# Performance work log

Measured on AMD Instinct MI355X. Metric: run time of the kernel, lower is better.

## Reference

```python
import jax, jax.numpy as jnp
import numpy as np

THRESH_SCALE = 0.05

def ste_ternary(w):
    # forward: quantize to {-1,0,+1}; backward: straight-through (identity)
    thr = THRESH_SCALE * jnp.mean(jnp.abs(w))
    q = jnp.where(w > thr, 1.0, jnp.where(w < -thr, -1.0, 0.0)).astype(w.dtype)
    return w + jax.lax.stop_gradient(q - w)

def setup_inputs() -> dict:
    key = jax.random.key(0)
    kx, kw = jax.random.split(key)
    x = jax.random.normal(kx, (8192, 4096), dtype=jnp.float32)
    weight = jax.random.normal(kw, (4096, 4096), dtype=jnp.float32) * 0.1
    return {"x": x, "weight": weight}

def reference(x, weight):
    w_t = ste_ternary(weight)          # [out, in] in {-1,0,+1}
    return x @ w_t.T                    # [tokens, out]
```

## Files before the change

kernel.cpp:

```cpp
#include <hip/hip_runtime.h>
#include <hip/hip_bf16.h>
#include <stdint.h>


typedef __attribute__((ext_vector_type(4))) int i32x4;

#define KDIM 4096
#define NDIM 4096

#define M_ROWS 8192
#define ABS_BLOCKS 1024

__device__ inline void gld_lds16(const void* g, void* l) {
  __builtin_amdgcn_global_load_lds(
      (__attribute__((address_space(1))) void*)g,
      (__attribute__((address_space(3))) void*)l,
      16, 0, 0);
}

__device__ inline int pack4(int a, int b, int c, int d) {
  return (a & 255) | ((b & 255) << 8) | ((c & 255) << 16) | (d << 24);
}

__device__ inline int q8(float v, float inv) {
  int q = __float2int_rn(v * inv);
  return q > 127 ? 127 : (q < -127 ? -127 : q);
}

__global__ __launch_bounds__(256) void prep_kernel(
    const float4* __restrict__ x, signed char* __restrict__ xq,
    float* __restrict__ steps, const float4* __restrict__ w, int wn4,
    double* __restrict__ sum) {
  if (blockIdx.x < M_ROWS) {
    const int row = blockIdx.x;
    const float4* xr = x + (size_t)row * 1024;
    float4 v[4];
    float amax = 0.0f;
#pragma unroll
    for (int j = 0; j < 4; ++j) {
      v[j] = xr[threadIdx.x + 256 * j];
      amax = fmaxf(amax, fmaxf(fmaxf(fabsf(v[j].x), fabsf(v[j].y)),
                               fmaxf(fabsf(v[j].z), fabsf(v[j].w))));
    }
#pragma unroll
    for (int off = 32; off > 0; off >>= 1)
      amax = fmaxf(amax, __shfl_down(amax, off, 64));
    __shared__ float wmax[4];
    const int lane = threadIdx.x & 63, wave = threadIdx.x >> 6;
    if (lane == 0) wmax[wave] = amax;
    __syncthreads();
    const float m = fmaxf(fmaxf(wmax[0], wmax[1]), fmaxf(wmax[2], wmax[3]));
    const float inv = m > 0.0f ? 127.0f / m : 0.0f;
    if (threadIdx.x == 0) steps[row] = m > 0.0f ? m / 127.0f : 0.0f;
    int* out = (int*)(xq + (size_t)row * 4096);
#pragma unroll
    for (int j = 0; j < 4; ++j) {
      out[threadIdx.x + 256 * j] = pack4(q8(v[j].x, inv), q8(v[j].y, inv),
                                         q8(v[j].z, inv), q8(v[j].w, inv));
    }
  } else {
    double s = 0.0;
    const int stride = ABS_BLOCKS * 256;
    for (int i = (blockIdx.x - M_ROWS) * 256 + threadIdx.x; i < wn4;
         i += stride) {
      float4 v = w[i];
      s += (double)((fabsf(v.x) + fabsf(v.y)) + (fabsf(v.z) + fabsf(v.w)));
    }
#pragma unroll
    for (int off = 32; off > 0; off >>= 1) s += __shfl_down(s, off, 64);
    __shared__ double wsum[4];
    const int lane = threadIdx.x & 63, wave = threadIdx.x >> 6;
    if (lane == 0) wsum[wave] = s;
    __syncthreads();
    if (threadIdx.x == 0) atomicAdd(sum, wsum[0] + wsum[1] + wsum[2] + wsum[3]);
  }
}

__global__ __launch_bounds__(256) void quant_kernel(
    const float4* __restrict__ w, const double* __restrict__ sum,
    int* __restrict__ q, int n4, double inv_n) {
  const float thr = (float)(0.05 * (*sum) * inv_n);
  const int stride = gridDim.x * blockDim.x;
  for (int i = blockIdx.x * blockDim.x + threadIdx.x; i < n4; i += stride) {
    float4 v = w[i];
    int a = v.x > thr ? 1 : (v.x < -thr ? -1 : 0);
    int b = v.y > thr ? 1 : (v.y < -thr ? -1 : 0);
    int c = v.z > thr ? 1 : (v.z < -thr ? -1 : 0);
    int d = v.w > thr ? 1 : (v.w < -thr ? -1 : 0);
    q[i] = pack4(a, b, c, d);
  }
}

#define MFMA_I8 __builtin_amdgcn_mfma_i32_16x16x64_i8

__global__ __launch_bounds__(512, 2) void gemm_i8_8p(
    const signed char* __restrict__ A, const signed char* __restrict__ B,
    const float* __restrict__ steps, float* __restrict__ C, int M) {
  __shared__ unsigned char lds[131072];

  const int tid = threadIdx.x;
  const int lane = tid & 63;
  const int w = tid >> 6;

  const int bm = blockIdx.y * 256;
  const int bn = blockIdx.x * 256;

  const int rL = lane >> 3;
  const int csw = (((lane & 7) ^ rL) << 4);
  const signed char* aBase = A + (size_t)(bm + w * 8 + rL) * KDIM + csw;
  const signed char* bBase = B + (size_t)(bn + w * 8 + rL) * KDIM + csw;
  unsigned char* const ldsA = lds;
  unsigned char* const ldsB = lds + 65536;

  const int fr = lane & 15;
  const int fk = (lane >> 4) * 16;
  const int xr = (lane & 7) << 4;
  const int cc0 = fk ^ xr;
  const int cc1 = (64 + fk) ^ xr;
  const int wm = (w >> 2) * 128;
  const int wn = (w & 3) * 64;
  const int aro = (wm + fr) * 128;
  const int bro = (wn + fr) * 128;

  i32x4 acc[8][4] = {};

  gld_lds16(bBase, ldsB + w * 1024);
  gld_lds16(bBase + (size_t)64 * KDIM, ldsB + 8192 + w * 1024);
  gld_lds16(bBase + (size_t)128 * KDIM, ldsB + 16384 + w * 1024);
  gld_lds16(bBase + (size_t)192 * KDIM, ldsB + 16384 + 8192 + w * 1024);
  gld_lds16(aBase, ldsA + w * 1024);
  gld_lds16(aBase + (size_t)128 * KDIM, ldsA + 16384 + w * 1024);
  gld_lds16(aBase + (size_t)64 * KDIM, ldsA + 8192 + w * 1024);
  gld_lds16(aBase + (size_t)192 * KDIM, ldsA + 16384 + 8192 + w * 1024);
  asm volatile("s_waitcnt vmcnt(2)" ::: "memory");
  __builtin_amdgcn_s_barrier();

  for (int t = 0; t < 32; ++t) {
    const int b = t & 1;
    const bool st = (t < 31);
    const unsigned char* Ab = ldsA + b * 32768;
    const unsigned char* Bb = ldsB + b * 32768;
    unsigned char* An = ldsA + (b ^ 1) * 32768;
    unsigned char* Bn = ldsB + (b ^ 1) * 32768;
    const signed char* aS = aBase + (size_t)(t + 1) * 128;
    const signed char* bS = bBase + (size_t)(t + 1) * 128;

    i32x4 bfr[4][2];

#pragma unroll
    for (int q = 0; q < 4; ++q) {
      if (q == 0) {
#pragma unroll
        for (int ni = 0; ni < 4; ++ni) {
          bfr[ni][0] = *(const i32x4*)(Bb + bro + ni * 2048 + cc0);
          bfr[ni][1] = *(const i32x4*)(Bb + bro + ni * 2048 + cc1);
        }
      }
      i32x4 a00 = *(const i32x4*)(Ab + aro + (2 * q) * 2048 + cc0);
      i32x4 a01 = *(const i32x4*)(Ab + aro + (2 * q) * 2048 + cc1);
      i32x4 a10 = *(const i32x4*)(Ab + aro + (2 * q + 1) * 2048 + cc0);
      i32x4 a11 = *(const i32x4*)(Ab + aro + (2 * q + 1) * 2048 + cc1);

      if (st) {
        if (q == 0) {
          gld_lds16(bS, Bn + w * 1024);
          gld_lds16(bS + (size_t)64 * KDIM, Bn + 8192 + w * 1024);
        } else if (q == 1) {
          gld_lds16(bS + (size_t)128 * KDIM, Bn + 16384 + w * 1024);
          gld_lds16(bS + (size_t)192 * KDIM, Bn + 16384 + 8192 + w * 1024);
        } else if (q == 2) {
          gld_lds16(aS, An + w * 1024);
          gld_lds16(aS + (size_t)128 * KDIM, An + 16384 + w * 1024);
        } else {
          gld_lds16(aS + (size_t)64 * KDIM, An + 8192 + w * 1024);
          gld_lds16(aS + (size_t)192 * KDIM, An + 16384 + 8192 + w * 1024);
        }
      }

      __builtin_amdgcn_s_barrier();
      asm volatile("s_waitcnt lgkmcnt(0)" ::: "memory");
      __builtin_amdgcn_s_setprio(1);
#pragma unroll
      for (int ni = 0; ni < 4; ++ni) {
        acc[2 * q][ni] = MFMA_I8(a00, bfr[ni][0], acc[2 * q][ni], 0, 0, 0);
        acc[2 * q][ni] = MFMA_I8(a01, bfr[ni][1], acc[2 * q][ni], 0, 0, 0);
        acc[2 * q + 1][ni] =
            MFMA_I8(a10, bfr[ni][0], acc[2 * q + 1][ni], 0, 0, 0);
        acc[2 * q + 1][ni] =
            MFMA_I8(a11, bfr[ni][1], acc[2 * q + 1][ni], 0, 0, 0);
      }
      __builtin_amdgcn_s_setprio(0);

      if (q == 1) {
        if (st)
          asm volatile("s_waitcnt vmcnt(4)" ::: "memory");
        else
          asm volatile("s_waitcnt vmcnt(0)" ::: "memory");
      }
      if (q == 3 && st)
        asm volatile("s_waitcnt vmcnt(2)" ::: "memory");
      __builtin_amdgcn_s_barrier();
    }
  }

  const int cn = lane & 15;
  const int cm = (lane >> 4) * 4;
  float stp[8][4];
#pragma unroll
  for (int mi = 0; mi < 8; ++mi)
#pragma unroll
    for (int r = 0; r < 4; ++r)
      stp[mi][r] = steps[bm + wm + mi * 16 + cm + r];
#pragma unroll
  for (int mi = 0; mi < 8; ++mi) {
#pragma unroll
    for (int ni = 0; ni < 4; ++ni) {
#pragma unroll
      for (int r = 0; r < 4; ++r) {
        const int m = bm + wm + mi * 16 + cm + r;
        const int n = bn + wn + ni * 16 + cn;
        C[(size_t)m * NDIM + n] = (float)acc[mi][ni][r] * stp[mi][r];
      }
    }
  }
}

extern "C" void kernel_launch(void* const* d_in, const int* in_sizes, int n_in,
                              void* d_out, int out_size, void* d_ws,
                              size_t ws_size, hipStream_t stream) {
  const float* x = (const float*)d_in[0];
  const float* w = (const float*)d_in[1];
  float* out = (float*)d_out;

  const int K = 4096;
  const int N = 4096;
  const int M = in_sizes[0] / K;
  const int NW = in_sizes[1];

  char* ws = (char*)d_ws;
  double* d_sum = (double*)ws;
  float* steps = (float*)(ws + 256);
  signed char* qb = (signed char*)(ws + 65536);
  signed char* xq = qb + (size_t)N * K;

  hipMemsetAsync(d_sum, 0, sizeof(double), stream);
  prep_kernel<<<M_ROWS + ABS_BLOCKS, 256, 0, stream>>>(
      (const float4*)x, xq, steps, (const float4*)w, NW / 4, d_sum);
  quant_kernel<<<2048, 256, 0, stream>>>((const float4*)w, d_sum, (int*)qb,
                                         NW / 4, 1.0 / NW);
  dim3 grid(N / 256, M / 256);
  gemm_i8_8p<<<grid, 512, 0, stream>>>(xq, qb, steps, out, M);
}
```

Before: 389.2 us.

## Halve GEMM K-tile to 64 with staggered A/B prefetch and smaller LDS

```diff
diff --git a/kernel.cpp b/kernel.cpp
--- a/kernel.cpp
+++ b/kernel.cpp
@@ -93,10 +93,10 @@
 
 #define MFMA_I8 __builtin_amdgcn_mfma_i32_16x16x64_i8
 
-__global__ __launch_bounds__(512, 2) void gemm_i8_8p(
+__global__ __launch_bounds__(512, 4) void gemm_i8_2b(
     const signed char* __restrict__ A, const signed char* __restrict__ B,
     const float* __restrict__ steps, float* __restrict__ C, int M) {
-  __shared__ unsigned char lds[131072];
+  __shared__ unsigned char lds[65536];
 
   const int tid = threadIdx.x;
   const int lane = tid & 63;
@@ -105,102 +105,87 @@
   const int bm = blockIdx.y * 256;
   const int bn = blockIdx.x * 256;
 
-  const int rL = lane >> 3;
-  const int csw = (((lane & 7) ^ rL) << 4);
-  const signed char* aBase = A + (size_t)(bm + w * 8 + rL) * KDIM + csw;
-  const signed char* bBase = B + (size_t)(bn + w * 8 + rL) * KDIM + csw;
+  const int srow = w * 16 + (lane >> 2);
+  const int srcsw = (((lane & 3) ^ ((lane >> 2) & 3) ^ ((lane >> 4) & 3)) << 4);
+  const signed char* aBase = A + (size_t)(bm + srow) * KDIM + srcsw;
+  const signed char* bBase = B + (size_t)(bn + srow) * KDIM + srcsw;
   unsigned char* const ldsA = lds;
-  unsigned char* const ldsB = lds + 65536;
+  unsigned char* const ldsB = lds + 32768;
 
   const int fr = lane & 15;
-  const int fk = (lane >> 4) * 16;
-  const int xr = (lane & 7) << 4;
-  const int cc0 = fk ^ xr;
-  const int cc1 = (64 + fk) ^ xr;
+  const int cc = (((lane >> 4) ^ (lane & 3) ^ ((lane >> 2) & 3)) << 4);
   const int wm = (w >> 2) * 128;
   const int wn = (w & 3) * 64;
-  const int aro = (wm + fr) * 128;
-  const int bro = (wn + fr) * 128;
+  const int aro = (wm + fr) * 64;
+  const int bro = (wn + fr) * 64;
 
   i32x4 acc[8][4] = {};
 
   gld_lds16(bBase, ldsB + w * 1024);
-  gld_lds16(bBase + (size_t)64 * KDIM, ldsB + 8192 + w * 1024);
-  gld_lds16(bBase + (size_t)128 * KDIM, ldsB + 16384 + w * 1024);
-  gld_lds16(bBase + (size_t)192 * KDIM, ldsB + 16384 + 8192 + w * 1024);
+  gld_lds16(bBase + (size_t)128 * KDIM, ldsB + 8192 + w * 1024);
   gld_lds16(aBase, ldsA + w * 1024);
-  gld_lds16(aBase + (size_t)128 * KDIM, ldsA + 16384 + w * 1024);
-  gld_lds16(aBase + (size_t)64 * KDIM, ldsA + 8192 + w * 1024);
-  gld_lds16(aBase + (size_t)192 * KDIM, ldsA + 16384 + 8192 + w * 1024);
+  gld_lds16(aBase + (size_t)128 * KDIM, ldsA + 8192 + w * 1024);
+  gld_lds16(bBase + 64, ldsB + 16384 + w * 1024);
+  gld_lds16(bBase + (size_t)128 * KDIM + 64, ldsB + 16384 + 8192 + w * 1024);
   asm volatile("s_waitcnt vmcnt(2)" ::: "memory");
   __builtin_amdgcn_s_barrier();
 
-  for (int t = 0; t < 32; ++t) {
+  for (int t = 0; t < 64; ++t) {
     const int b = t & 1;
-    const bool st = (t < 31);
-    const unsigned char* Ab = ldsA + b * 32768;
-    const unsigned char* Bb = ldsB + b * 32768;
-    unsigned char* An = ldsA + (b ^ 1) * 32768;
-    unsigned char* Bn = ldsB + (b ^ 1) * 32768;
-    const signed char* aS = aBase + (size_t)(t + 1) * 128;
-    const signed char* bS = bBase + (size_t)(t + 1) * 128;
-
-    i32x4 bfr[4][2];
-
-#pragma unroll
-    for (int q = 0; q < 4; ++q) {
-      if (q == 0) {
-#pragma unroll
-        for (int ni = 0; ni < 4; ++ni) {
-          bfr[ni][0] = *(const i32x4*)(Bb + bro + ni * 2048 + cc0);
-          bfr[ni][1] = *(const i32x4*)(Bb + bro + ni * 2048 + cc1);
-        }
-      }
-      i32x4 a00 = *(const i32x4*)(Ab + aro + (2 * q) * 2048 + cc0);
-      i32x4 a01 = *(const i32x4*)(Ab + aro + (2 * q) * 2048 + cc1);
-      i32x4 a10 = *(const i32x4*)(Ab + aro + (2 * q + 1) * 2048 + cc0);
-      i32x4 a11 = *(const i32x4*)(Ab + aro + (2 * q + 1) * 2048 + cc1);
-
-      if (st) {
-        if (q == 0) {
-          gld_lds16(bS, Bn + w * 1024);
-          gld_lds16(bS + (size_t)64 * KDIM, Bn + 8192 + w * 1024);
-        } else if (q == 1) {
-          gld_lds16(bS + (size_t)128 * KDIM, Bn + 16384 + w * 1024);
-          gld_lds16(bS + (size_t)192 * KDIM, Bn + 16384 + 8192 + w * 1024);
-        } else if (q == 2) {
-          gld_lds16(aS, An + w * 1024);
-          gld_lds16(aS + (size_t)128 * KDIM, An + 16384 + w * 1024);
-        } else {
-          gld_lds16(aS + (size_t)64 * KDIM, An + 8192 + w * 1024);
-          gld_lds16(aS + (size_t)192 * KDIM, An + 16384 + 8192 + w * 1024);
-        }
-      }
-
-      __builtin_amdgcn_s_barrier();
-      asm volatile("s_waitcnt lgkmcnt(0)" ::: "memory");
-      __builtin_amdgcn_s_setprio(1);
-#pragma unroll
-      for (int ni = 0; ni < 4; ++ni) {
-        acc[2 * q][ni] = MFMA_I8(a00, bfr[ni][0], acc[2 * q][ni], 0, 0, 0);
-        acc[2 * q][ni] = MFMA_I8(a01, bfr[ni][1], acc[2 * q][ni], 0, 0, 0);
-        acc[2 * q + 1][ni] =
-            MFMA_I8(a10, bfr[ni][0], acc[2 * q + 1][ni], 0, 0, 0);
-        acc[2 * q + 1][ni] =
-            MFMA_I8(a11, bfr[ni][1], acc[2 * q + 1][ni], 0, 0, 0);
-      }
-      __builtin_amdgcn_s_setprio(0);
-
-      if (q == 1) {
-        if (st)
-          asm volatile("s_waitcnt vmcnt(4)" ::: "memory");
-        else
-          asm volatile("s_waitcnt vmcnt(0)" ::: "memory");
-      }
-      if (q == 3 && st)
-        asm volatile("s_waitcnt vmcnt(2)" ::: "memory");
-      __builtin_amdgcn_s_barrier();
-    }
+    const unsigned char* Ab = ldsA + b * 16384;
+    const unsigned char* Bb = ldsB + b * 16384;
+
+    i32x4 bfr[4], af[4];
+#pragma unroll
+    for (int ni = 0; ni < 4; ++ni)
+      bfr[ni] = *(const i32x4*)(Bb + bro + ni * 1024 + cc);
+#pragma unroll
+    for (int i = 0; i < 4; ++i)
+      af[i] = *(const i32x4*)(Ab + aro + i * 1024 + cc);
+
+    if (t + 1 < 64) {
+      unsigned char* An = ldsA + ((t + 1) & 1) * 16384;
+      const signed char* aS = aBase + (size_t)(t + 1) * 64;
+      gld_lds16(aS, An + w * 1024);
+      gld_lds16(aS + (size_t)128 * KDIM, An + 8192 + w * 1024);
+    }
+
+    __builtin_amdgcn_s_barrier();
+    asm volatile("s_waitcnt lgkmcnt(0)" ::: "memory");
+    __builtin_amdgcn_s_setprio(1);
+#pragma unroll
+    for (int i = 0; i < 4; ++i)
+#pragma unroll
+      for (int ni = 0; ni < 4; ++ni)
+        acc[i][ni] = MFMA_I8(af[i], bfr[ni], acc[i][ni], 0, 0, 0);
+    __builtin_amdgcn_s_setprio(0);
+    __builtin_amdgcn_s_barrier();
+
+#pragma unroll
+    for (int i = 0; i < 4; ++i)
+      af[i] = *(const i32x4*)(Ab + aro + (4 + i) * 1024 + cc);
+
+    if (t + 2 < 64) {
+      const signed char* bS = bBase + (size_t)(t + 2) * 64;
+      gld_lds16(bS, ldsB + b * 16384 + w * 1024);
+      gld_lds16(bS + (size_t)128 * KDIM, ldsB + b * 16384 + 8192 + w * 1024);
+    }
+
+    __builtin_amdgcn_s_barrier();
+    asm volatile("s_waitcnt lgkmcnt(0)" ::: "memory");
+    __builtin_amdgcn_s_setprio(1);
+#pragma unroll
+    for (int i = 0; i < 4; ++i)
+#pragma unroll
+      for (int ni = 0; ni < 4; ++ni)
+        acc[4 + i][ni] = MFMA_I8(af[i], bfr[ni], acc[4 + i][ni], 0, 0, 0);
+    __builtin_amdgcn_s_setprio(0);
+
+    if (t <= 61)
+      asm volatile("s_waitcnt vmcnt(2)" ::: "memory");
+    else if (t == 62)
+      asm volatile("s_waitcnt vmcnt(0)" ::: "memory");
+    __builtin_amdgcn_s_barrier();
   }
 
   const int cn = lane & 15;
@@ -249,5 +234,5 @@
   quant_kernel<<<2048, 256, 0, stream>>>((const float4*)w, d_sum, (int*)qb,
                                          NW / 4, 1.0 / NW);
   dim3 grid(N / 256, M / 256);
-  gemm_i8_8p<<<grid, 512, 0, stream>>>(xq, qb, steps, out, M);
-}
+  gemm_i8_2b<<<grid, 512, 0, stream>>>(xq, qb, steps, out, M);
+}
```

Measured after the change: 1.451 ms. 273% more time.

## Restructure int8 GEMM k-loop to one barrier per tile with bulk fragment loads

Applied to the files above, without the earlier changes.

```diff
diff --git a/kernel.cpp b/kernel.cpp
--- a/kernel.cpp
+++ b/kernel.cpp
@@ -93,7 +93,7 @@
 
 #define MFMA_I8 __builtin_amdgcn_mfma_i32_16x16x64_i8
 
-__global__ __launch_bounds__(512, 2) void gemm_i8_8p(
+__global__ __launch_bounds__(512, 2) void gemm_i8_1b(
     const signed char* __restrict__ A, const signed char* __restrict__ B,
     const float* __restrict__ steps, float* __restrict__ C, int M) {
   __shared__ unsigned char lds[131072];
@@ -129,77 +129,72 @@
   gld_lds16(bBase + (size_t)128 * KDIM, ldsB + 16384 + w * 1024);
   gld_lds16(bBase + (size_t)192 * KDIM, ldsB + 16384 + 8192 + w * 1024);
   gld_lds16(aBase, ldsA + w * 1024);
+  gld_lds16(aBase + (size_t)64 * KDIM, ldsA + 8192 + w * 1024);
   gld_lds16(aBase + (size_t)128 * KDIM, ldsA + 16384 + w * 1024);
-  gld_lds16(aBase + (size_t)64 * KDIM, ldsA + 8192 + w * 1024);
   gld_lds16(aBase + (size_t)192 * KDIM, ldsA + 16384 + 8192 + w * 1024);
-  asm volatile("s_waitcnt vmcnt(2)" ::: "memory");
+  asm volatile("s_waitcnt vmcnt(0)" ::: "memory");
   __builtin_amdgcn_s_barrier();
+  __builtin_amdgcn_sched_barrier(0);
 
   for (int t = 0; t < 32; ++t) {
     const int b = t & 1;
-    const bool st = (t < 31);
     const unsigned char* Ab = ldsA + b * 32768;
     const unsigned char* Bb = ldsB + b * 32768;
-    unsigned char* An = ldsA + (b ^ 1) * 32768;
-    unsigned char* Bn = ldsB + (b ^ 1) * 32768;
-    const signed char* aS = aBase + (size_t)(t + 1) * 128;
-    const signed char* bS = bBase + (size_t)(t + 1) * 128;
-
-    i32x4 bfr[4][2];
-
-#pragma unroll
-    for (int q = 0; q < 4; ++q) {
-      if (q == 0) {
-#pragma unroll
-        for (int ni = 0; ni < 4; ++ni) {
-          bfr[ni][0] = *(const i32x4*)(Bb + bro + ni * 2048 + cc0);
-          bfr[ni][1] = *(const i32x4*)(Bb + bro + ni * 2048 + cc1);
-        }
-      }
-      i32x4 a00 = *(const i32x4*)(Ab + aro + (2 * q) * 2048 + cc0);
-      i32x4 a01 = *(const i32x4*)(Ab + aro + (2 * q) * 2048 + cc1);
-      i32x4 a10 = *(const i32x4*)(Ab + aro + (2 * q + 1) * 2048 + cc0);
-      i32x4 a11 = *(const i32x4*)(Ab + aro + (2 * q + 1) * 2048 + cc1);
-
-      if (st) {
-        if (q == 0) {
-          gld_lds16(bS, Bn + w * 1024);
-          gld_lds16(bS + (size_t)64 * KDIM, Bn + 8192 + w * 1024);
-        } else if (q == 1) {
-          gld_lds16(bS + (size_t)128 * KDIM, Bn + 16384 + w * 1024);
-          gld_lds16(bS + (size_t)192 * KDIM, Bn + 16384 + 8192 + w * 1024);
-        } else if (q == 2) {
-          gld_lds16(aS, An + w * 1024);
-          gld_lds16(aS + (size_t)128 * KDIM, An + 16384 + w * 1024);
-        } else {
-          gld_lds16(aS + (size_t)64 * KDIM, An + 8192 + w * 1024);
-          gld_lds16(aS + (size_t)192 * KDIM, An + 16384 + 8192 + w * 1024);
-        }
-      }
-
+
+    i32x4 bfr[4][2], af0[8], af1[8];
+#pragma unroll
+    for (int ni = 0; ni < 4; ++ni) {
+      bfr[ni][0] = *(const i32x4*)(Bb + bro + ni * 2048 + cc0);
+      bfr[ni][1] = *(const i32x4*)(Bb + bro + ni * 2048 + cc1);
+    }
+#pragma unroll
+    for (int m = 0; m < 8; ++m)
+      af0[m] = *(const i32x4*)(Ab + aro + m * 2048 + cc0);
+
+    if (t + 1 < 32) {
+      unsigned char* An = ldsA + (b ^ 1) * 32768;
+      unsigned char* Bn = ldsB + (b ^ 1) * 32768;
+      const signed char* aS = aBase + (size_t)(t + 1) * 128;
+      const signed char* bS = bBase + (size_t)(t + 1) * 128;
+      gld_lds16(bS, Bn + w * 1024);
+      gld_lds16(bS + (size_t)64 * KDIM, Bn + 8192 + w * 1024);
+      gld_lds16(bS + (size_t)128 * KDIM, Bn + 16384 + w * 1024);
+      gld_lds16(bS + (size_t)192 * KDIM, Bn + 16384 + 8192 + w * 1024);
+      gld_lds16(aS, An + w * 1024);
+      gld_lds16(aS + (size_t)64 * KDIM, An + 8192 + w * 1024);
+      gld_lds16(aS + (size_t)128 * KDIM, An + 16384 + w * 1024);
+      gld_lds16(aS + (size_t)192 * KDIM, An + 16384 + 8192 + w * 1024);
+    }
+
+    __builtin_amdgcn_s_setprio(1);
+#pragma unroll
+    for (int m = 0; m < 4; ++m)
+#pragma unroll
+      for (int ni = 0; ni < 4; ++ni)
+        acc[m][ni] = MFMA_I8(af0[m], bfr[ni][0], acc[m][ni], 0, 0, 0);
+    __builtin_amdgcn_s_setprio(0);
+
+#pragma unroll
+    for (int m = 0; m < 8; ++m)
+      af1[m] = *(const i32x4*)(Ab + aro + m * 2048 + cc1);
+
+    __builtin_amdgcn_s_setprio(1);
+#pragma unroll
+    for (int m = 4; m < 8; ++m)
+#pragma unroll
+      for (int ni = 0; ni < 4; ++ni)
+        acc[m][ni] = MFMA_I8(af0[m], bfr[ni][0], acc[m][ni], 0, 0, 0);
+#pragma unroll
+    for (int m = 0; m < 8; ++m)
+#pragma unroll
+      for (int ni = 0; ni < 4; ++ni)
+        acc[m][ni] = MFMA_I8(af1[m], bfr[ni][1], acc[m][ni], 0, 0, 0);
+    __builtin_amdgcn_s_setprio(0);
+
+    if (t + 1 < 32) {
+      asm volatile("s_waitcnt vmcnt(0)" ::: "memory");
       __builtin_amdgcn_s_barrier();
-      asm volatile("s_waitcnt lgkmcnt(0)" ::: "memory");
-      __builtin_amdgcn_s_setprio(1);
-#pragma unroll
-      for (int ni = 0; ni < 4; ++ni) {
-        acc[2 * q][ni] = MFMA_I8(a00, bfr[ni][0], acc[2 * q][ni], 0, 0, 0);
-        acc[2 * q][ni] = MFMA_I8(a01, bfr[ni][1], acc[2 * q][ni], 0, 0, 0);
-        acc[2 * q + 1][ni] =
-            MFMA_I8(a10, bfr[ni][0], acc[2 * q + 1][ni], 0, 0, 0);
-        acc[2 * q + 1][ni] =
-            MFMA_I8(a11, bfr[ni][1], acc[2 * q + 1][ni], 0, 0, 0);
-      }
-      __builtin_amdgcn_s_setprio(0);
-
-      if (q == 1) {
-        if (st)
-          asm volatile("s_waitcnt vmcnt(4)" ::: "memory");
-        else
-          asm volatile("s_waitcnt vmcnt(0)" ::: "memory");
-      }
-      if (q == 3 && st)
-        asm volatile("s_waitcnt vmcnt(2)" ::: "memory");
-      __builtin_amdgcn_s_barrier();
+      __builtin_amdgcn_sched_barrier(0);
     }
   }
 
@@ -249,5 +244,5 @@
   quant_kernel<<<2048, 256, 0, stream>>>((const float4*)w, d_sum, (int*)qb,
                                          NW / 4, 1.0 / NW);
   dim3 grid(N / 256, M / 256);
-  gemm_i8_8p<<<grid, 512, 0, stream>>>(xq, qb, steps, out, M);
-}
+  gemm_i8_1b<<<grid, 512, 0, stream>>>(xq, qb, steps, out, M);
+}
```

After: 387.2 us. Within noise of the previous version (-0.5%).
